# Kernel optimization log

Measured on AMD Instinct MI355X. Metric: run time of the kernel, lower is better.

The kernel has to match this reference:

```python
import jax, jax.numpy as jnp
import numpy as np

B, S, E, H, C = 16, 2048, 128, 768, 457


def setup_inputs() -> dict:
    key = jax.random.key(0)
    ks = jax.random.split(key, 8)
    hidden_states = jax.random.normal(ks[0], (B, S, H), dtype=jnp.float32)
    field_labels = jax.random.randint(ks[1], (B, S), 0, C, dtype=jnp.int64) if jax.config.jax_enable_x64 else jax.random.randint(ks[1], (B, S), 0, C, dtype=jnp.int32)
    label_masks = jax.random.randint(ks[2], (B, S), 0, 2, dtype=jnp.int32)
    entities_attr = jax.random.randint(ks[3], (B, E), 0, C, dtype=jnp.int32)
    entities_list = (jax.random.uniform(ks[4], (B, S, E)) < 0.05).astype(jnp.int32)
    entities_len = jnp.maximum(entities_list.sum(axis=1), 1).astype(jnp.int32)  # (B, E)
    entities_mask = jax.random.randint(ks[5], (B, E), 0, 2).astype(bool)
    W = jax.random.normal(ks[6], (C, H), dtype=jnp.float32) * 0.02
    b = jax.random.normal(ks[7], (C,), dtype=jnp.float32) * 0.02
    return {"hidden_states": hidden_states, "field_labels": field_labels,
            "label_masks": label_masks, "entities_attr": entities_attr,
            "entities_list": entities_list, "entities_len": entities_len,
            "entities_mask": entities_mask, "W": W, "b": b}


def reference(hidden_states, field_labels, label_masks, entities_attr,
              entities_list, entities_len, entities_mask, W, b):
    # Entity mean-pool: torch does (B,E,S,H) expand*mul->sum; algebraically a bmm.
    dt = hidden_states.dtype
    ent_hidden = jnp.einsum('bsh,bse->beh', hidden_states, entities_list.astype(dt))
    ent_hidden = ent_hidden / entities_len.astype(dt)[..., None]        # (B,E,H)
    mc_logits = jnp.einsum('beh,ch->bec', ent_hidden, W) + b             # (B,E,C)
    # masked CrossEntropyLoss (mean over selected entities)
    logp = jax.nn.log_softmax(mc_logits, axis=-1)
    nll = -jnp.take_along_axis(logp, entities_attr[..., None].astype(jnp.int32), axis=-1)[..., 0]
    m = entities_mask.astype(dt)
    mask_loss = (nll * m).sum() / m.sum()
    return mask_loss
```

## Files before the change

kernel.cpp:

```cpp
#include <hip/hip_runtime.h>
#include <hip/hip_bf16.h>
#include <cstdint>
#include <cstddef>

constexpr int Bn = 16, Sn = 2048, En = 128, Hn = 768, Cn = 457;
constexpr int NP = 512;
using f32x4  = __attribute__((ext_vector_type(4))) float;
using bf16x8 = __attribute__((ext_vector_type(8))) short;

static __device__ inline unsigned short f2bf(float x) {
  __hip_bfloat16 b = __float2bfloat16(x);
  return *reinterpret_cast<unsigned short*>(&b);
}

__global__ __launch_bounds__(256) void pack_k(
    const int* __restrict__ el, unsigned int* __restrict__ pk)
{
  const int l = threadIdx.x & 63;
  const int gw = blockIdx.x * 4 + (threadIdx.x >> 6);
  #pragma unroll 4
  for (int j = 0; j < 32; ++j) {
    const int tok = gw * 32 + j;
    const int v0 = el[(size_t)tok * 128 + l];
    const int v1 = el[(size_t)tok * 128 + 64 + l];
    const unsigned long long b0 = __ballot(v0 != 0);
    const unsigned long long b1 = __ballot(v1 != 0);
    if (l == 0) {
      ulonglong2 w; w.x = b0; w.y = b1;
      *reinterpret_cast<ulonglong2*>(pk + (size_t)tok * 4) = w;
    }
  }
}

constexpr int PBN = 64, PBK = 32, PLD = 40;
constexpr int SCH = 4, SLEN = Sn / SCH, PNK = SLEN / PBK;
__global__ __launch_bounds__(512, 6) void pool_k(
    const float* __restrict__ hidden,
    const unsigned int* __restrict__ pk,
    float* __restrict__ entp)
{
  const int b = blockIdx.x, n0 = blockIdx.y * PBN, sc = blockIdx.z;
  const int s0 = sc * SLEN;
  const int tid = threadIdx.x, l = tid & 63, wv = tid >> 6;
  const int wm = wv >> 2, wn = wv & 3;

  __shared__ unsigned short As[2][En][PLD];
  __shared__ unsigned short Bs[2][PBN][PLD];
  __shared__ unsigned int   PKs[SLEN * 4];

  {
    const uint4* src = reinterpret_cast<const uint4*>(pk + ((size_t)b * Sn + s0) * 4);
    reinterpret_cast<uint4*>(PKs)[tid] = src[tid];
  }

  const float* hb = hidden + ((size_t)b * Sn + s0) * Hn + n0;
  const int half = l >> 5, bit = l & 31;

  auto loadh = [&](int kk, float (&f)[4]) {
    const int sb = kk * PBK + wv * 4;
    f[0] = hb[(size_t)(sb + 0) * Hn + l];
    f[1] = hb[(size_t)(sb + 1) * Hn + l];
    f[2] = hb[(size_t)(sb + 2) * Hn + l];
    f[3] = hb[(size_t)(sb + 3) * Hn + l];
  };

  auto stage = [&](int kk, int bsel, const float (&f)[4]) {
    const int sb = kk * PBK + wv * 4;
    unsigned int w0[4], w1[4];
    #pragma unroll
    for (int i = 0; i < 4; ++i) {
      w0[i] = PKs[(sb + i) * 4 + half];
      w1[i] = PKs[(sb + i) * 4 + 2 + half];
    }
    auto sel = [&](unsigned int w, int hi) -> unsigned int {
      return ((w >> bit) & 1u) ? (hi ? 0x3F800000u : 0x3F80u) : 0u;
    };
    uint2 da, db, dh;
    da.x = sel(w0[0], 0) | sel(w0[1], 1);
    da.y = sel(w0[2], 0) | sel(w0[3], 1);
    db.x = sel(w1[0], 0) | sel(w1[1], 1);
    db.y = sel(w1[2], 0) | sel(w1[3], 1);
    dh.x = (unsigned int)f2bf(f[0]) | ((unsigned int)f2bf(f[1]) << 16);
    dh.y = (unsigned int)f2bf(f[2]) | ((unsigned int)f2bf(f[3]) << 16);
    *reinterpret_cast<uint2*>(&As[bsel][l]     [wv * 4]) = da;
    *reinterpret_cast<uint2*>(&As[bsel][l + 64][wv * 4]) = db;
    *reinterpret_cast<uint2*>(&Bs[bsel][l]     [wv * 4]) = dh;
  };

  f32x4 acc[4] = {};
  const int rl = l & 15, kr = (l >> 4) * 8;

  auto mfma_step = [&](int cur) {
    const bf16x8 bfr = *reinterpret_cast<const bf16x8*>(&Bs[cur][wn * 16 + rl][kr]);
    #pragma unroll
    for (int mi = 0; mi < 4; ++mi) {
      const bf16x8 afr =
          *reinterpret_cast<const bf16x8*>(&As[cur][wm * 64 + mi * 16 + rl][kr]);
      acc[mi] = __builtin_amdgcn_mfma_f32_16x16x32_bf16(afr, bfr, acc[mi], 0, 0, 0);
    }
  };

  float pf[3][4];
  loadh(0, pf[0]);
  loadh(1, pf[1]);
  __syncthreads();
  stage(0, 0, pf[0]);
  __syncthreads();

  #pragma unroll
  for (int k = 0; k < PNK; ++k) {
    if (k + 2 < PNK) loadh(k + 2, pf[(k + 2) % 3]);
    mfma_step(k & 1);
    if (k + 1 < PNK) stage(k + 1, (k + 1) & 1, pf[(k + 1) % 3]);
    __syncthreads();
  }

  float* dst = entp + (size_t)sc * Bn * En * Hn;
  const int rg = (l >> 4) * 4;
  const int col = n0 + wn * 16 + rl;
  #pragma unroll
  for (int mi = 0; mi < 4; ++mi) {
    #pragma unroll
    for (int r = 0; r < 4; ++r) {
      const int e = wm * 64 + mi * 16 + rg + r;
      dst[(size_t)(b * En + e) * Hn + col] = acc[mi][r];
    }
  }
}

__global__ __launch_bounds__(256) void finalize_k(
    const float* __restrict__ entp, const int* __restrict__ elen,
    unsigned short* __restrict__ entbf)
{
  const int be = blockIdx.x, tid = threadIdx.x;
  const float inv = 1.0f / (float)elen[be];
  constexpr size_t PS = (size_t)Bn * En * Hn;
  const float* src = entp + (size_t)be * Hn;
  unsigned short* dst = entbf + (size_t)be * Hn;
  #pragma unroll
  for (int j = 0; j < 3; ++j) {
    const int h = tid + j * 256;
    const float v = src[h] + src[h + PS] + src[h + 2 * PS] + src[h + 3 * PS];
    dst[h] = f2bf(v * inv);
  }
}

__global__ __launch_bounds__(256) void cast_w_k(
    const float* __restrict__ Wm, unsigned short* __restrict__ wbf)
{
  const int c = blockIdx.x;
  const int tid = threadIdx.x;
  unsigned short* dst = wbf + (size_t)c * Hn;
  if (c < Cn) {
    const float* src = Wm + (size_t)c * Hn;
    #pragma unroll
    for (int j = 0; j < 3; ++j) dst[tid + j * 256] = f2bf(src[tid + j * 256]);
  } else {
    #pragma unroll
    for (int j = 0; j < 3; ++j) dst[tid + j * 256] = 0;
  }
}

constexpr int BM = 128, BN = 64, BK = 32, LDP = BK + 24;
__global__ __launch_bounds__(256) void gemm_k(
    const unsigned short* __restrict__ A,
    const unsigned short* __restrict__ Bm,
    float* __restrict__ Cm)
{
  __shared__ unsigned short As[BM][LDP];
  __shared__ unsigned short Bs[BN][LDP];
  const int bm = blockIdx.x, bn = blockIdx.y;
  const int tid = threadIdx.x, lane = tid & 63, wv = tid >> 6;
  const int wm = wv >> 1, wn = wv & 1;

  f32x4 acc[4][2] = {};

  for (int k0 = 0; k0 < Hn; k0 += BK) {
    #pragma unroll
    for (int i = 0; i < 2; ++i) {
      const int idx = tid + i * 256;
      const int r = idx >> 2, kc = (idx & 3) * 8;
      const unsigned short* src = A + (size_t)(bm * BM + r) * Hn + k0 + kc;
      *reinterpret_cast<ulonglong2*>(&As[r][kc]) =
          *reinterpret_cast<const ulonglong2*>(src);
    }
    {
      const int r = tid >> 2, kc = (tid & 3) * 8;
      const unsigned short* src = Bm + (size_t)(bn * BN + r) * Hn + k0 + kc;
      *reinterpret_cast<ulonglong2*>(&Bs[r][kc]) =
          *reinterpret_cast<const ulonglong2*>(src);
    }
    __syncthreads();

    const int kr = (lane >> 4) * 8, rl = lane & 15;
    bf16x8 af[4], bf[2];
    #pragma unroll
    for (int mi = 0; mi < 4; ++mi)
      af[mi] = *reinterpret_cast<const bf16x8*>(&As[wm * 64 + mi * 16 + rl][kr]);
    #pragma unroll
    for (int ni = 0; ni < 2; ++ni)
      bf[ni] = *reinterpret_cast<const bf16x8*>(&Bs[wn * 32 + ni * 16 + rl][kr]);
    #pragma unroll
    for (int mi = 0; mi < 4; ++mi)
      #pragma unroll
      for (int ni = 0; ni < 2; ++ni)
        acc[mi][ni] = __builtin_amdgcn_mfma_f32_16x16x32_bf16(
            af[mi], bf[ni], acc[mi][ni], 0, 0, 0);
    __syncthreads();
  }

  const int cl = lane & 15, rg = (lane >> 4) * 4;
  #pragma unroll
  for (int mi = 0; mi < 4; ++mi)
    #pragma unroll
    for (int ni = 0; ni < 2; ++ni) {
      const int col = bn * BN + wn * 32 + ni * 16 + cl;
      #pragma unroll
      for (int r = 0; r < 4; ++r) {
        const int row = bm * BM + wm * 64 + mi * 16 + rg + r;
        Cm[(size_t)row * NP + col] = acc[mi][ni][r];
      }
    }
}

__global__ __launch_bounds__(256) void ce_k(
    const float* __restrict__ logits,
    const float* __restrict__ bv,
    const int* __restrict__ attr,
    const unsigned char* __restrict__ emask,
    float* __restrict__ nll)
{
  const int wv = threadIdx.x >> 6, lane = threadIdx.x & 63;
  const int be = blockIdx.x * 4 + wv;
  if (!emask[be]) { if (lane == 0) nll[be] = 0.f; return; }
  const float* row = logits + (size_t)be * NP;

  float mx = -3.4e38f;
  for (int i = lane; i < Cn; i += 64) mx = fmaxf(mx, row[i] + bv[i]);
  #pragma unroll
  for (int o = 32; o; o >>= 1) mx = fmaxf(mx, __shfl_xor(mx, o, 64));
  float sm = 0.f;
  for (int i = lane; i < Cn; i += 64) sm += __expf(row[i] + bv[i] - mx);
  #pragma unroll
  for (int o = 32; o; o >>= 1) sm += __shfl_xor(sm, o, 64);
  if (lane == 0) {
    const int tg = attr[be];
    nll[be] = mx + logf(sm) - (row[tg] + bv[tg]);
  }
}

__global__ __launch_bounds__(256) void reduce_k(
    const float* __restrict__ nll,
    const unsigned char* __restrict__ emask,
    float* __restrict__ out)
{
  const int tid = threadIdx.x;
  float s = 0.f, c = 0.f;
  for (int i = tid; i < Bn * En; i += 256) {
    s += nll[i];
    c += (float)emask[i];
  }
  #pragma unroll
  for (int o = 32; o; o >>= 1) {
    s += __shfl_xor(s, o, 64);
    c += __shfl_xor(c, o, 64);
  }
  __shared__ float ws_[4], wc_[4];
  const int wave = tid >> 6, lane = tid & 63;
  if (lane == 0) { ws_[wave] = s; wc_[wave] = c; }
  __syncthreads();
  if (tid == 0) {
    out[0] = (ws_[0] + ws_[1] + ws_[2] + ws_[3]) /
             (wc_[0] + wc_[1] + wc_[2] + wc_[3]);
  }
}

extern "C" void kernel_launch(void* const* d_in, const int* in_sizes, int n_in,
                              void* d_out, int out_size, void* d_ws, size_t ws_size,
                              hipStream_t stream) {
  const float* hidden        = (const float*)d_in[0];
  const int* attr            = (const int*)d_in[3];
  const int* el              = (const int*)d_in[4];
  const int* elen            = (const int*)d_in[5];
  const unsigned char* emask = (const unsigned char*)d_in[6];
  const float* Wm            = (const float*)d_in[7];
  const float* bv            = (const float*)d_in[8];

  unsigned short* entbf = (unsigned short*)d_ws;
  unsigned short* wbf   = entbf + (size_t)Bn * En * Hn;
  float* logits = (float*)(wbf + (size_t)NP * Hn);
  float* nll    = logits + (size_t)Bn * En * NP;
  unsigned int* pkbuf = (unsigned int*)(nll + Bn * En);
  float* entp   = (float*)(pkbuf + (size_t)Bn * Sn * 4);

  hipLaunchKernelGGL(pack_k, dim3(256), dim3(256), 0, stream, el, pkbuf);
  hipLaunchKernelGGL(pool_k, dim3(Bn, Hn / PBN, SCH), dim3(512), 0, stream,
                     hidden, pkbuf, entp);
  hipLaunchKernelGGL(finalize_k, dim3(Bn * En), dim3(256), 0, stream,
                     entp, elen, entbf);
  hipLaunchKernelGGL(cast_w_k, dim3(NP), dim3(256), 0, stream, Wm, wbf);
  hipLaunchKernelGGL(gemm_k, dim3(Bn * En / BM, NP / BN), dim3(256), 0, stream,
                     entbf, wbf, logits);
  hipLaunchKernelGGL(ce_k, dim3(Bn * En / 4), dim3(256), 0, stream,
                     logits, bv, attr, emask, nll);
  hipLaunchKernelGGL(reduce_k, dim3(1), dim3(256), 0, stream,
                     nll, emask, (float*)d_out);
}
```

Measured before the change: 65.58 us.

## Transpose packed entity bitmask and build MFMA A-fragments directly in registers

The packed entity membership bits are stored word-major (4 x S per batch), so pool_k builds the 0/1 bf16 A fragments straight from LDS bitmask words inside the MFMA step. This removes the As shared-memory staging buffer and its writes and reads. Partial sums are now written as bf16 instead of fp32, which halves the traffic into finalize_k; finalize_k reads packed pairs with 384 threads. pack_k uses more blocks with fewer tokens each. The cost is some precision loss from rounding partial sums to bf16, plus extra ALU work per MFMA to expand the bits.

After: 63.49 us. 1.03x faster.

```diff
diff --git a/kernel.cpp b/kernel.cpp
--- a/kernel.cpp
+++ b/kernel.cpp
@@ -12,22 +12,34 @@
   __hip_bfloat16 b = __float2bfloat16(x);
   return *reinterpret_cast<unsigned short*>(&b);
 }
+static __device__ inline float bflo(unsigned int u) {
+  unsigned int v = u << 16;
+  return *reinterpret_cast<float*>(&v);
+}
+static __device__ inline float bfhi(unsigned int u) {
+  unsigned int v = u & 0xFFFF0000u;
+  return *reinterpret_cast<float*>(&v);
+}
 
 __global__ __launch_bounds__(256) void pack_k(
-    const int* __restrict__ el, unsigned int* __restrict__ pk)
+    const int* __restrict__ el, unsigned int* __restrict__ pk2)
 {
   const int l = threadIdx.x & 63;
   const int gw = blockIdx.x * 4 + (threadIdx.x >> 6);
-  #pragma unroll 4
-  for (int j = 0; j < 32; ++j) {
-    const int tok = gw * 32 + j;
+  #pragma unroll 8
+  for (int j = 0; j < 8; ++j) {
+    const int tok = gw * 8 + j;
+    const int b = tok >> 11, s = tok & 2047;
     const int v0 = el[(size_t)tok * 128 + l];
     const int v1 = el[(size_t)tok * 128 + 64 + l];
     const unsigned long long b0 = __ballot(v0 != 0);
     const unsigned long long b1 = __ballot(v1 != 0);
     if (l == 0) {
-      ulonglong2 w; w.x = b0; w.y = b1;
-      *reinterpret_cast<ulonglong2*>(pk + (size_t)tok * 4) = w;
+      unsigned int* p = pk2 + (size_t)b * 4 * Sn + s;
+      p[0]          = (unsigned int)b0;
+      p[Sn]         = (unsigned int)(b0 >> 32);
+      p[2 * Sn]     = (unsigned int)b1;
+      p[3 * Sn]     = (unsigned int)(b1 >> 32);
     }
   }
 }
@@ -36,25 +48,25 @@
 constexpr int SCH = 4, SLEN = Sn / SCH, PNK = SLEN / PBK;
 __global__ __launch_bounds__(512, 6) void pool_k(
     const float* __restrict__ hidden,
-    const unsigned int* __restrict__ pk,
-    float* __restrict__ entp)
+    const unsigned int* __restrict__ pk2,
+    unsigned short* __restrict__ entp)
 {
   const int b = blockIdx.x, n0 = blockIdx.y * PBN, sc = blockIdx.z;
   const int s0 = sc * SLEN;
   const int tid = threadIdx.x, l = tid & 63, wv = tid >> 6;
   const int wm = wv >> 2, wn = wv & 3;
 
-  __shared__ unsigned short As[2][En][PLD];
   __shared__ unsigned short Bs[2][PBN][PLD];
-  __shared__ unsigned int   PKs[SLEN * 4];
+  __shared__ unsigned int   PK2[4 * SLEN];
 
   {
-    const uint4* src = reinterpret_cast<const uint4*>(pk + ((size_t)b * Sn + s0) * 4);
-    reinterpret_cast<uint4*>(PKs)[tid] = src[tid];
+    const int w = tid >> 7, off = (tid & 127) * 4;
+    const uint4 v = *reinterpret_cast<const uint4*>(
+        pk2 + (size_t)b * 4 * Sn + (size_t)w * Sn + s0 + off);
+    *reinterpret_cast<uint4*>(&PK2[w * SLEN + off]) = v;
   }
 
   const float* hb = hidden + ((size_t)b * Sn + s0) * Hn + n0;
-  const int half = l >> 5, bit = l & 31;
 
   auto loadh = [&](int kk, float (&f)[4]) {
     const int sb = kk * PBK + wv * 4;
@@ -64,39 +76,41 @@
     f[3] = hb[(size_t)(sb + 3) * Hn + l];
   };
 
-  auto stage = [&](int kk, int bsel, const float (&f)[4]) {
-    const int sb = kk * PBK + wv * 4;
-    unsigned int w0[4], w1[4];
-    #pragma unroll
-    for (int i = 0; i < 4; ++i) {
-      w0[i] = PKs[(sb + i) * 4 + half];
-      w1[i] = PKs[(sb + i) * 4 + 2 + half];
-    }
-    auto sel = [&](unsigned int w, int hi) -> unsigned int {
-      return ((w >> bit) & 1u) ? (hi ? 0x3F800000u : 0x3F80u) : 0u;
-    };
-    uint2 da, db, dh;
-    da.x = sel(w0[0], 0) | sel(w0[1], 1);
-    da.y = sel(w0[2], 0) | sel(w0[3], 1);
-    db.x = sel(w1[0], 0) | sel(w1[1], 1);
-    db.y = sel(w1[2], 0) | sel(w1[3], 1);
+  auto stage_b = [&](int bsel, const float (&f)[4]) {
+    uint2 dh;
     dh.x = (unsigned int)f2bf(f[0]) | ((unsigned int)f2bf(f[1]) << 16);
     dh.y = (unsigned int)f2bf(f[2]) | ((unsigned int)f2bf(f[3]) << 16);
-    *reinterpret_cast<uint2*>(&As[bsel][l]     [wv * 4]) = da;
-    *reinterpret_cast<uint2*>(&As[bsel][l + 64][wv * 4]) = db;
-    *reinterpret_cast<uint2*>(&Bs[bsel][l]     [wv * 4]) = dh;
+    *reinterpret_cast<uint2*>(&Bs[bsel][l][wv * 4]) = dh;
   };
 
   f32x4 acc[4] = {};
-  const int rl = l & 15, kr = (l >> 4) * 8;
-
-  auto mfma_step = [&](int cur) {
-    const bf16x8 bfr = *reinterpret_cast<const bf16x8*>(&Bs[cur][wn * 16 + rl][kr]);
-    #pragma unroll
-    for (int mi = 0; mi < 4; ++mi) {
-      const bf16x8 afr =
-          *reinterpret_cast<const bf16x8*>(&As[cur][wm * 64 + mi * 16 + rl][kr]);
-      acc[mi] = __builtin_amdgcn_mfma_f32_16x16x32_bf16(afr, bfr, acc[mi], 0, 0, 0);
+  const int rl = l & 15, q = l >> 4, kr = q * 8;
+
+  auto mfma_step = [&](int k, int cur) {
+    const int sbase = k * PBK + kr;
+    const bf16x8 bfr =
+        *reinterpret_cast<const bf16x8*>(&Bs[cur][wn * 16 + rl][kr]);
+    #pragma unroll
+    for (int mp = 0; mp < 2; ++mp) {
+      const int w = wm * 2 + mp;
+      const uint4 u0 = *reinterpret_cast<const uint4*>(&PK2[w * SLEN + sbase]);
+      const uint4 u1 = *reinterpret_cast<const uint4*>(&PK2[w * SLEN + sbase + 4]);
+      #pragma unroll
+      for (int mh = 0; mh < 2; ++mh) {
+        const int bi = mh * 16 + rl;
+        bf16x8 afr;
+        unsigned int* ap = reinterpret_cast<unsigned int*>(&afr);
+        ap[0] = (((u0.x >> bi) & 1u) ? 0x3F80u : 0u) |
+                (((u0.y >> bi) & 1u) ? 0x3F800000u : 0u);
+        ap[1] = (((u0.z >> bi) & 1u) ? 0x3F80u : 0u) |
+                (((u0.w >> bi) & 1u) ? 0x3F800000u : 0u);
+        ap[2] = (((u1.x >> bi) & 1u) ? 0x3F80u : 0u) |
+                (((u1.y >> bi) & 1u) ? 0x3F800000u : 0u);
+        ap[3] = (((u1.z >> bi) & 1u) ? 0x3F80u : 0u) |
+                (((u1.w >> bi) & 1u) ? 0x3F800000u : 0u);
+        acc[mp * 2 + mh] = __builtin_amdgcn_mfma_f32_16x16x32_bf16(
+            afr, bfr, acc[mp * 2 + mh], 0, 0, 0);
+      }
     }
   };
 
@@ -104,45 +118,49 @@
   loadh(0, pf[0]);
   loadh(1, pf[1]);
   __syncthreads();
-  stage(0, 0, pf[0]);
+  stage_b(0, pf[0]);
   __syncthreads();
 
   #pragma unroll
   for (int k = 0; k < PNK; ++k) {
     if (k + 2 < PNK) loadh(k + 2, pf[(k + 2) % 3]);
-    mfma_step(k & 1);
-    if (k + 1 < PNK) stage(k + 1, (k + 1) & 1, pf[(k + 1) % 3]);
+    mfma_step(k, k & 1);
+    if (k + 1 < PNK) stage_b((k + 1) & 1, pf[(k + 1) % 3]);
     __syncthreads();
   }
 
-  float* dst = entp + (size_t)sc * Bn * En * Hn;
-  const int rg = (l >> 4) * 4;
+  unsigned short* dst = entp + (size_t)sc * Bn * En * Hn;
+  const int rg = q * 4;
   const int col = n0 + wn * 16 + rl;
   #pragma unroll
   for (int mi = 0; mi < 4; ++mi) {
     #pragma unroll
     for (int r = 0; r < 4; ++r) {
       const int e = wm * 64 + mi * 16 + rg + r;
-      dst[(size_t)(b * En + e) * Hn + col] = acc[mi][r];
-    }
-  }
-}
-
-__global__ __launch_bounds__(256) void finalize_k(
-    const float* __restrict__ entp, const int* __restrict__ elen,
+      dst[(size_t)(b * En + e) * Hn + col] = f2bf(acc[mi][r]);
+    }
+  }
+}
+
+__global__ __launch_bounds__(384) void finalize_k(
+    const unsigned short* __restrict__ entp, const int* __restrict__ elen,
     unsigned short* __restrict__ entbf)
 {
-  const int be = blockIdx.x, tid = threadIdx.x;
+  const int be = blockIdx.x, t = threadIdx.x;
   const float inv = 1.0f / (float)elen[be];
-  constexpr size_t PS = (size_t)Bn * En * Hn;
-  const float* src = entp + (size_t)be * Hn;
-  unsigned short* dst = entbf + (size_t)be * Hn;
-  #pragma unroll
-  for (int j = 0; j < 3; ++j) {
-    const int h = tid + j * 256;
-    const float v = src[h] + src[h + PS] + src[h + 2 * PS] + src[h + 3 * PS];
-    dst[h] = f2bf(v * inv);
-  }
+  constexpr size_t PSu = (size_t)Bn * En * Hn / 2;
+  const unsigned int* src =
+      reinterpret_cast<const unsigned int*>(entp) + (size_t)be * (Hn / 2) + t;
+  float lo = 0.f, hi = 0.f;
+  #pragma unroll
+  for (int p = 0; p < SCH; ++p) {
+    const unsigned int u = src[p * PSu];
+    lo += bflo(u);
+    hi += bfhi(u);
+  }
+  const unsigned int out = (unsigned int)f2bf(lo * inv) |
+                           ((unsigned int)f2bf(hi * inv) << 16);
+  reinterpret_cast<unsigned int*>(entbf)[(size_t)be * (Hn / 2) + t] = out;
 }
 
 __global__ __launch_bounds__(256) void cast_w_k(
@@ -290,13 +308,14 @@
   unsigned short* wbf   = entbf + (size_t)Bn * En * Hn;
   float* logits = (float*)(wbf + (size_t)NP * Hn);
   float* nll    = logits + (size_t)Bn * En * NP;
-  unsigned int* pkbuf = (unsigned int*)(nll + Bn * En);
-  float* entp   = (float*)(pkbuf + (size_t)Bn * Sn * 4);
-
-  hipLaunchKernelGGL(pack_k, dim3(256), dim3(256), 0, stream, el, pkbuf);
+  unsigned int* pk2buf = (unsigned int*)(nll + Bn * En);
+  unsigned short* entp =
+      (unsigned short*)(pk2buf + (size_t)Bn * 4 * Sn);
+
+  hipLaunchKernelGGL(pack_k, dim3(1024), dim3(256), 0, stream, el, pk2buf);
   hipLaunchKernelGGL(pool_k, dim3(Bn, Hn / PBN, SCH), dim3(512), 0, stream,
-                     hidden, pkbuf, entp);
-  hipLaunchKernelGGL(finalize_k, dim3(Bn * En), dim3(256), 0, stream,
+                     hidden, pk2buf, entp);
+  hipLaunchKernelGGL(finalize_k, dim3(Bn * En), dim3(384), 0, stream,
                      entp, elen, entbf);
   hipLaunchKernelGGL(cast_w_k, dim3(NP), dim3(256), 0, stream, Wm, wbf);
   hipLaunchKernelGGL(gemm_k, dim3(Bn * En / BM, NP / BN), dim3(256), 0, stream,
```
